# Kernel optimization log

Measured on AMD Instinct MI355X. Metric: run time of the kernel, lower is better.

The kernel has to match this reference:

```python
import jax, jax.numpy as jnp
import numpy as np

N, E = 50000, 800000
IN = OUT = 128
T, R, H = 4, 6, 8
DK = OUT // H


def setup_inputs() -> dict:
    key = jax.random.key(0)
    ks = iter(jax.random.split(key, 24))
    nk = lambda: next(ks)
    return {
        "node_inp": jax.random.normal(nk(), (N, IN), jnp.float32),
        "node_type": jax.random.randint(nk(), (N,), 0, T),
        "edge_index": jax.random.randint(nk(), (2, E), 0, N),
        "edge_type": jax.random.randint(nk(), (E,), 0, R),
        "edge_sign": jax.random.randint(nk(), (E,), -2, 2),
        "edge_distance": jax.random.uniform(nk(), (E,), jnp.float32, 0.0, 2e5),
        "Wq": jax.random.normal(nk(), (T, IN, OUT), jnp.float32) / np.float32(np.sqrt(IN)),
        "bq": jnp.zeros((T, OUT), jnp.float32),
        "Wk": jax.random.normal(nk(), (T, IN, OUT), jnp.float32) / np.float32(np.sqrt(IN)),
        "bk": jnp.zeros((T, OUT), jnp.float32),
        "Wv": jax.random.normal(nk(), (T, IN, OUT), jnp.float32) / np.float32(np.sqrt(IN)),
        "bv": jnp.zeros((T, OUT), jnp.float32),
        "rel_q": jax.random.normal(nk(), (R, H, DK), jnp.float32) * 0.2,
        "rel_k": jax.random.normal(nk(), (R, H, DK), jnp.float32) * 0.2,
        "rel_v": jax.random.normal(nk(), (R, H, DK), jnp.float32) * 0.2,
        "sign_k_neutral": jnp.ones((H, DK), jnp.float32),
        "sign_v_neutral": jnp.ones((H, DK), jnp.float32),
        "rel_bias": jnp.zeros((R, H), jnp.float32),
        "dist_alpha": jnp.asarray(0.5, jnp.float32),
        "dist_tau": jnp.asarray(100000.0, jnp.float32),
        "skip": jnp.ones((T,), jnp.float32),
        "ln_gamma": jnp.ones((T, OUT), jnp.float32),
        "ln_beta": jnp.zeros((T, OUT), jnp.float32),
    }


def reference(node_inp, node_type, edge_index, edge_type, edge_sign, edge_distance,
              Wq, bq, Wk, bk, Wv, bv, rel_q, rel_k, rel_v,
              sign_k_neutral, sign_v_neutral, rel_bias, dist_alpha, dist_tau,
              skip, ln_gamma, ln_beta):
    n = node_inp.shape[0]
    src, dst = edge_index[0], edge_index[1]

    # edge_sign normalization: anything < -1 or == 0 -> -2 (neutral), else clamp to {-1, 1}
    es = jnp.where((edge_sign < -1) | (edge_sign == 0), -2, jnp.clip(edge_sign, -1, 1))
    sign_idx = jnp.where(es == -1, 0, jnp.where(es == 1, 1, 2))  # [E]

    # per-type Q/K/V projections, then select by node_type
    idx = jnp.arange(n)
    Q = (jnp.einsum('ni,tio->tno', node_inp, Wq) + bq[:, None, :])[node_type, idx]
    K = (jnp.einsum('ni,tio->tno', node_inp, Wk) + bk[:, None, :])[node_type, idx]
    V = (jnp.einsum('ni,tio->tno', node_inp, Wv) + bv[:, None, :])[node_type, idx]
    Q = Q.reshape(n, H, DK); K = K.reshape(n, H, DK); V = V.reshape(n, H, DK)

    sign_k_all = jnp.concatenate([-jnp.ones((1, H, DK), Q.dtype), jnp.ones((1, H, DK), Q.dtype), sign_k_neutral[None]], 0)
    sign_v_all = jnp.concatenate([-jnp.ones((1, H, DK), Q.dtype), jnp.ones((1, H, DK), Q.dtype), sign_v_neutral[None]], 0)

    q_eff = Q[dst] * rel_q[edge_type]                        # [E,H,DK]
    k_eff = K[src] * rel_k[edge_type] * sign_k_all[sign_idx]  # [E,H,DK]
    v_eff = V[src] * rel_v[edge_type] * sign_v_all[sign_idx]  # [E,H,DK]

    scores = (q_eff * k_eff).sum(-1) / np.float32(np.sqrt(DK))  # [E,H]
    scores = scores + rel_bias[edge_type]
    phi = dist_alpha * jnp.exp(-edge_distance / (dist_tau + 1e-9))
    scores = scores + phi[:, None]

    # destination-grouped softmax over edges
    m = jax.ops.segment_max(scores, dst, num_segments=n)      # [N,H]
    ex = jnp.exp(scores - m[dst])
    Z = jax.ops.segment_sum(ex, dst, num_segments=n)          # [N,H]
    attn = ex / (Z[dst] + 1e-9)                               # [E,H]

    msg = (v_eff * attn[..., None]).reshape(-1, OUT)          # [E,OUT]
    out = jax.ops.segment_sum(msg, dst, num_segments=n)       # [N,OUT]

    alpha = jax.nn.sigmoid(skip)[node_type][:, None]          # [N,1]
    mix = alpha * out + (1.0 - alpha) * node_inp
    mu = mix.mean(-1, keepdims=True)
    var = ((mix - mu) ** 2).mean(-1, keepdims=True)
    normed = (mix - mu) / jnp.sqrt(var + 1e-5)
    return normed * ln_gamma[node_type] + ln_beta[node_type]
```

## Files before the change

### kernel.cpp

```cpp
#include <hip/hip_runtime.h>

#define N_NODES 50000
#define N_EDGES 800000
#define DIM 128
#define NT 4
#define NR 6
#define NH 8
#define NBLK_SCAN ((N_NODES + 255) / 256)
#define NBLK2 ((N_NODES + 1023) / 1024)
#define NTILE_ROW 3129
#define NPAD_MAX (NTILE_ROW * 16)

#define XCVT_N (N_NODES * DIM / 4)
#define WT_N   (NT * 3 * DIM * DIM)
#define WCB_N  (24 * 32)
#define PREP_TOTAL (XCVT_N + WT_N + WCB_N)
#define PREP_BLOCKS ((PREP_TOTAL + 255) / 256)
#define HIST_BLOCKS (N_EDGES / 256)
#define A_PREP_BASE NBLK_SCAN
#define A_HIST_BASE (NBLK_SCAN + PREP_BLOCKS)
#define A_BLOCKS (A_HIST_BASE + HIST_BLOCKS)

typedef __attribute__((ext_vector_type(8))) short bf16x8;
typedef __attribute__((ext_vector_type(4))) float f32x4;

__device__ __forceinline__ unsigned short f2bf(float f) {
    unsigned int u = __float_as_uint(f);
    return (unsigned short)((u + 0x7fffu + ((u >> 16) & 1u)) >> 16);
}
__device__ __forceinline__ float blo(unsigned int u) { return __uint_as_float(u << 16); }
__device__ __forceinline__ float bhi(unsigned int u) { return __uint_as_float(u & 0xffff0000u); }

__device__ __forceinline__ int sign_index(int s) {
    if (s < -1 || s == 0) return 2;
    return (s == -1) ? 0 : 1;
}

__global__ __launch_bounds__(256) void k_A(
    const int* __restrict__ ntype, int* __restrict__ bhist, int* __restrict__ opad,
    const float* __restrict__ x,
    const float* __restrict__ Wq, const float* __restrict__ Wk, const float* __restrict__ Wv,
    const float* __restrict__ rel_q, const float* __restrict__ rel_k,
    const float* __restrict__ rel_v,
    const float* __restrict__ skn, const float* __restrict__ svn,
    unsigned short* __restrict__ xb, unsigned short* __restrict__ Wt,
    uint4* __restrict__ wcb,
    const int* __restrict__ ei, int* __restrict__ cnt, int* __restrict__ posw)
{
    int blk = blockIdx.x;
    if (blk < NBLK_SCAN) {
        __shared__ int h[NT];
        if (threadIdx.x < NT) h[threadIdx.x] = 0;
        __syncthreads();
        int n = blk * 256 + threadIdx.x;
        if (n < N_NODES) atomicAdd(&h[ntype[n]], 1);
        if (n < NPAD_MAX) opad[n] = -1;
        __syncthreads();
        if (threadIdx.x < NT) bhist[blk * NT + threadIdx.x] = h[threadIdx.x];
        return;
    }
    if (blk < A_HIST_BASE) {
        int i = (blk - A_PREP_BASE) * 256 + threadIdx.x;
        if (i < XCVT_N) {
            float4 v = ((const float4*)x)[i];
            ushort4 o;
            o.x = f2bf(v.x); o.y = f2bf(v.y); o.z = f2bf(v.z); o.w = f2bf(v.w);
            ((ushort4*)xb)[i] = o;
        } else if (i < XCVT_N + WT_N) {
            int j = i - XCVT_N;
            int in = j & 127;
            int b2 = j >> 7;
            int out = b2 & 127;
            int ts = b2 >> 7;
            int sel = ts % 3, t = ts / 3;
            const float* W = sel == 0 ? Wq : (sel == 1 ? Wk : Wv);
            Wt[j] = f2bf(W[((size_t)t * DIM + in) * DIM + out]);
        } else if (i < PREP_TOTAL) {
            int j = i - XCVT_N - WT_N;
            int p = j & 31;
            int cmb = j >> 5;
            int et = cmb & 7, sidx = cmb >> 3;
            if (et < NR) {
                int h2 = p >> 2;
                float wk[4], wv[4];
                #pragma unroll
                for (int q = 0; q < 4; ++q) {
                    int o = 4 * p + q;
                    int rb = (et * NH + h2) * 16 + (o & 15);
                    float sgk = sidx == 0 ? -1.f : (sidx == 1 ? 1.f : skn[o]);
                    float sgv = sidx == 0 ? -1.f : (sidx == 1 ? 1.f : svn[o]);
                    wk[q] = rel_q[rb] * rel_k[rb] * sgk * 0.25f;
                    wv[q] = rel_v[rb] * sgv;
                }
                uint4 u;
                u.x = (unsigned)f2bf(wk[0]) | ((unsigned)f2bf(wk[1]) << 16);
                u.y = (unsigned)f2bf(wv[0]) | ((unsigned)f2bf(wv[1]) << 16);
                u.z = (unsigned)f2bf(wk[2]) | ((unsigned)f2bf(wk[3]) << 16);
                u.w = (unsigned)f2bf(wv[2]) | ((unsigned)f2bf(wv[3]) << 16);
                wcb[cmb * 32 + p] = u;
            }
        }
        return;
    }
    int e = (blk - A_HIST_BASE) * 256 + threadIdx.x;
    if (e < N_EDGES) posw[e] = atomicAdd(&cnt[ei[N_EDGES + e]], 1);
}

__global__ __launch_bounds__(1024) void k_B(
    const int* __restrict__ bhist, int* __restrict__ bbase, int* __restrict__ pb_g,
    const int* __restrict__ cnt, int* __restrict__ offs, int* __restrict__ bsum)
{
    int tid = threadIdx.x;
    if (blockIdx.x == 0) {
        __shared__ int s[1024];
        __shared__ int pb[NT + 1];
        int t = tid / NBLK_SCAN;
        int b = tid - t * NBLK_SCAN;
        int v = (tid < NT * NBLK_SCAN) ? bhist[b * NT + t] : 0;
        s[tid] = v;
        __syncthreads();
        for (int d = 1; d < 1024; d <<= 1) {
            int add = (tid >= d) ? s[tid - d] : 0;
            __syncthreads();
            s[tid] += add;
            __syncthreads();
        }
        if (tid == 0) {
            int acc = 0;
            for (int tt = 0; tt < NT; ++tt) {
                pb[tt] = acc;
                int tot = s[(tt + 1) * NBLK_SCAN - 1] - (tt ? s[tt * NBLK_SCAN - 1] : 0);
                acc += ((tot + 15) >> 4) << 4;
            }
            pb[NT] = acc;
        }
        __syncthreads();
        if (tid < NT * NBLK_SCAN) {
            int excl = s[tid] - v;
            int base_t = t ? s[t * NBLK_SCAN - 1] : 0;
            bbase[b * NT + t] = pb[t] + (excl - base_t);
        }
        if (tid <= NT) pb_g[tid] = pb[tid];
        return;
    }
    int sb = blockIdx.x - 1;
    __shared__ int s[1024];
    int i = sb * 1024 + tid;
    int v = (i < N_NODES) ? cnt[i] : 0;
    s[tid] = v;
    __syncthreads();
    for (int d = 1; d < 1024; d <<= 1) {
        int add = (tid >= d) ? s[tid - d] : 0;
        __syncthreads();
        s[tid] += add;
        __syncthreads();
    }
    if (i < N_NODES) offs[i] = s[tid] - v;
    if (tid == 1023) bsum[sb] = s[1023];
}

__global__ __launch_bounds__(256) void k_C(
    const int* __restrict__ ntype, const int* __restrict__ bbase, int* __restrict__ order_pad,
    const int* __restrict__ bsum, int* __restrict__ bofs, int* __restrict__ offs)
{
    int blk = blockIdx.x;
    if (blk < NBLK_SCAN) {
        __shared__ int cur[NT];
        if (threadIdx.x < NT) cur[threadIdx.x] = bbase[blk * NT + threadIdx.x];
        __syncthreads();
        int n = blk * 256 + threadIdx.x;
        if (n < N_NODES) {
            int t = ntype[n];
            int pos = atomicAdd(&cur[t], 1);
            order_pad[pos] = n;
        }
        return;
    }
    __shared__ int s[256];
    int t = threadIdx.x;
    int v = (t < NBLK2) ? bsum[t] : 0;
    s[t] = v;
    __syncthreads();
    for (int d = 1; d < 256; d <<= 1) {
        int add = (t >= d) ? s[t - d] : 0;
        __syncthreads();
        s[t] += add;
        __syncthreads();
    }
    if (t < NBLK2) {
        int b = s[t] - v;
        bofs[t] = b;
        if (t == NBLK2 - 1) offs[N_NODES] = N_EDGES - b;
    }
}

__global__ __launch_bounds__(256) void k_D(
    const unsigned short* __restrict__ xb, const unsigned short* __restrict__ Wt,
    const int* __restrict__ order_pad, const int* __restrict__ pb_g,
    const float* __restrict__ bq, const float* __restrict__ bk, const float* __restrict__ bv,
    float* __restrict__ Qf, unsigned short* __restrict__ KVu,
    const int* __restrict__ ei, const int* __restrict__ etype,
    const int* __restrict__ esign, const float* __restrict__ edist,
    const float* __restrict__ dalpha, const float* __restrict__ dtau,
    const int* __restrict__ offs, const int* __restrict__ bofs,
    const int* __restrict__ posw, int2* __restrict__ edata)
{
    int b = blockIdx.x;
    if (b >= NTILE_ROW) {
        int e = (b - NTILE_ROW) * 256 + threadIdx.x;
        if (e >= N_EDGES) return;
        int dst = ei[N_EDGES + e];
        int pos = offs[dst] + bofs[dst >> 10] + posw[e];
        int cmb = sign_index(esign[e]) * 8 + etype[e];
        float phi = dalpha[0] * __expf(-edist[e] / (dtau[0] + 1e-9f));
        edata[pos] = make_int2(ei[e] | (cmb << 16), __float_as_int(phi));
        return;
    }
    int row0 = b * 16;
    if (row0 >= pb_g[NT]) return;
    int t = (row0 >= pb_g[3]) ? 3 : (row0 >= pb_g[2]) ? 2 : (row0 >= pb_g[1]) ? 1 : 0;
    int wave = threadIdx.x >> 6, lane = threadIdx.x & 63;
    int arow = row0 + (lane & 15);
    int nidA = order_pad[arow];
    const unsigned short* xrow = xb + (size_t)(nidA < 0 ? 0 : nidA) * DIM;
    int ko = (lane >> 4) * 8;
    bf16x8 afrag[4];
    #pragma unroll
    for (int kt = 0; kt < 4; ++kt) afrag[kt] = *(const bf16x8*)(xrow + kt * 32 + ko);

    #pragma unroll
    for (int g = 0; g < 6; ++g) {
        int ocol = g * 64 + wave * 16 + (lane & 15);
        int sel = ocol >> 7, wcol = ocol & 127;
        const unsigned short* wrow = Wt + ((size_t)(t * 3 + sel) * DIM + wcol) * DIM;
        f32x4 acc = {0.f, 0.f, 0.f, 0.f};
        #pragma unroll
        for (int kt = 0; kt < 4; ++kt) {
            bf16x8 bfr = *(const bf16x8*)(wrow + kt * 32 + ko);
            acc = __builtin_amdgcn_mfma_f32_16x16x32_bf16(afrag[kt], bfr, acc, 0, 0, 0);
        }
        const float* bias_p = sel == 0 ? bq : (sel == 1 ? bk : bv);
        float bias = bias_p[t * DIM + wcol];
        #pragma unroll
        for (int r = 0; r < 4; ++r) {
            int drow = row0 + (lane >> 4) * 4 + r;
            int nid = order_pad[drow];
            if (nid < 0) continue;
            float v = acc[r] + bias;
            if (sel == 0) Qf[(size_t)nid * DIM + wcol] = v;
            else KVu[(size_t)nid * 256 + (wcol >> 1) * 4 + (wcol & 1) + (sel == 2 ? 2 : 0)] = f2bf(v);
        }
    }
}

__global__ __launch_bounds__(256) void k_attn(
    const float4* __restrict__ Qf4, const uint4* __restrict__ KV,
    const uint4* __restrict__ WCB,
    const float* __restrict__ x, const int* __restrict__ ntype,
    const int* __restrict__ offs, const int* __restrict__ bofs,
    const int2* __restrict__ edata,
    const float* __restrict__ rbias, const float* __restrict__ skip,
    const float* __restrict__ gmm, const float* __restrict__ bta,
    float* __restrict__ out)
{
    __shared__ float rb_s[NR * NH];
    if (threadIdx.x < NR * NH) rb_s[threadIdx.x] = rbias[threadIdx.x];
    __syncthreads();
    const int wave = threadIdx.x >> 6, lane = threadIdx.x & 63;
    const int n = blockIdx.x * 4 + wave;
    const int p = lane & 31;
    const int hi = lane >> 5;
    const int h = p >> 2;
    const int beg = offs[n] + bofs[n >> 10];
    const int end = offs[n + 1] + bofs[(n + 1) >> 10];

    const float4 q4 = Qf4[(size_t)n * 32 + p];

    float Z = 0.f, a0 = 0.f, a1 = 0.f, a2 = 0.f, a3 = 0.f;

    auto process = [&](int2 r) {
        int src = r.x & 0xffff;
        unsigned cmb = ((unsigned)r.x) >> 16;
        uint4 kv = KV[(size_t)src * 32 + p];
        uint4 w = WCB[cmb * 32 + p];
        float pp = (q4.x * blo(w.x)) * blo(kv.x);
        pp = fmaf(q4.y * bhi(w.x), bhi(kv.x), pp);
        pp = fmaf(q4.z * blo(w.z), blo(kv.z), pp);
        pp = fmaf(q4.w * bhi(w.z), bhi(kv.z), pp);
        pp += __shfl_xor(pp, 1, 4);
        pp += __shfl_xor(pp, 2, 4);
        float ex = __expf(pp + rb_s[(cmb & 7) * NH + h] + __int_as_float(r.y));
        Z += ex;
        a0 = fmaf(blo(kv.y) * blo(w.y), ex, a0);
        a1 = fmaf(bhi(kv.y) * bhi(w.y), ex, a1);
        a2 = fmaf(blo(kv.w) * blo(w.w), ex, a2);
        a3 = fmaf(bhi(kv.w) * bhi(w.w), ex, a3);
    };

    int rem = end - beg;
    int j = beg;
    if (rem >= 4) {
        int2 r0 = edata[j + hi];
        int2 r1 = edata[j + 2 + hi];
        while (true) {
            int2 c0 = r0, c1 = r1;
            j += 4; rem -= 4;
            if (rem >= 4) { r0 = edata[j + hi]; r1 = edata[j + 2 + hi]; }
            process(c0);
            process(c1);
            if (rem < 4) break;
        }
    }
    while (rem >= 2) {
        int2 c = edata[j + hi];
        process(c);
        j += 2; rem -= 2;
    }
    if (rem) {
        int2 r = edata[j];
        int src = r.x & 0xffff;
        unsigned cmb = ((unsigned)r.x) >> 16;
        uint4 kv = KV[(size_t)src * 32 + p];
        uint4 w = WCB[cmb * 32 + p];
        float pp = (q4.x * blo(w.x)) * blo(kv.x);
        pp = fmaf(q4.y * bhi(w.x), bhi(kv.x), pp);
        pp = fmaf(q4.z * blo(w.z), blo(kv.z), pp);
        pp = fmaf(q4.w * bhi(w.z), bhi(kv.z), pp);
        pp += __shfl_xor(pp, 1, 4);
        pp += __shfl_xor(pp, 2, 4);
        float ex = __expf(pp + rb_s[(cmb & 7) * NH + h] + __int_as_float(r.y));
        ex = hi ? 0.f : ex;
        Z += ex;
        a0 = fmaf(blo(kv.y) * blo(w.y), ex, a0);
        a1 = fmaf(bhi(kv.y) * bhi(w.y), ex, a1);
        a2 = fmaf(blo(kv.w) * blo(w.w), ex, a2);
        a3 = fmaf(bhi(kv.w) * bhi(w.w), ex, a3);
    }

    Z  += __shfl_xor(Z, 32, 64);
    a0 += __shfl_xor(a0, 32, 64);
    a1 += __shfl_xor(a1, 32, 64);
    a2 += __shfl_xor(a2, 32, 64);
    a3 += __shfl_xor(a3, 32, 64);

    float rz = 1.f / (Z + 1e-9f);
    int t = ntype[n];
    float alpha = 1.f / (1.f + __expf(-skip[t]));
    float4 x4 = ((const float4*)x)[(size_t)n * 32 + p];
    float m0 = fmaf(alpha, a0 * rz - x4.x, x4.x);
    float m1 = fmaf(alpha, a1 * rz - x4.y, x4.y);
    float m2 = fmaf(alpha, a2 * rz - x4.z, x4.z);
    float m3 = fmaf(alpha, a3 * rz - x4.w, x4.w);

    float s = (m0 + m1) + (m2 + m3);
    float s2 = fmaf(m0, m0, m1 * m1) + fmaf(m2, m2, m3 * m3);
    #pragma unroll
    for (int d = 32; d >= 1; d >>= 1) {
        s += __shfl_xor(s, d, 64);
        s2 += __shfl_xor(s2, d, 64);
    }
    float mu = s * (1.f / (2 * DIM));
    float var = s2 * (1.f / (2 * DIM)) - mu * mu;
    float rstd = rsqrtf(var + 1e-5f);
    if (hi == 0) {
        float4 g4 = ((const float4*)gmm)[t * 32 + p];
        float4 b4 = ((const float4*)bta)[t * 32 + p];
        float4 o4;
        o4.x = (m0 - mu) * rstd * g4.x + b4.x;
        o4.y = (m1 - mu) * rstd * g4.y + b4.y;
        o4.z = (m2 - mu) * rstd * g4.z + b4.z;
        o4.w = (m3 - mu) * rstd * g4.w + b4.w;
        ((float4*)out)[(size_t)n * 32 + p] = o4;
    }
}

extern "C" void kernel_launch(void* const* d_in, const int* in_sizes, int n_in,
                              void* d_out, int out_size, void* d_ws, size_t ws_size,
                              hipStream_t stream) {
    const float* x      = (const float*)d_in[0];
    const int*   ntype  = (const int*)d_in[1];
    const int*   ei     = (const int*)d_in[2];
    const int*   etype  = (const int*)d_in[3];
    const int*   esign  = (const int*)d_in[4];
    const float* edist  = (const float*)d_in[5];
    const float* Wq     = (const float*)d_in[6];
    const float* bq     = (const float*)d_in[7];
    const float* Wk     = (const float*)d_in[8];
    const float* bk     = (const float*)d_in[9];
    const float* Wv     = (const float*)d_in[10];
    const float* bv     = (const float*)d_in[11];
    const float* rel_q  = (const float*)d_in[12];
    const float* rel_k  = (const float*)d_in[13];
    const float* rel_v  = (const float*)d_in[14];
    const float* skn    = (const float*)d_in[15];
    const float* svn    = (const float*)d_in[16];
    const float* rbias  = (const float*)d_in[17];
    const float* dalpha = (const float*)d_in[18];
    const float* dtau   = (const float*)d_in[19];
    const float* skip   = (const float*)d_in[20];
    const float* gmm    = (const float*)d_in[21];
    const float* bta    = (const float*)d_in[22];
    float* out = (float*)d_out;

    char* ws = (char*)d_ws;
    float*          Qf     = (float*)         (ws + 0);
    unsigned short* KVu    = (unsigned short*)(ws + 25600000);
    unsigned short* xb     = (unsigned short*)(ws + 51200000);
    unsigned short* Wt     = (unsigned short*)(ws + 64000000);
    uint4*          wcb    = (uint4*)         (ws + 64500000);
    int*            cnt    = (int*)           (ws + 64600000);
    int*            offs   = (int*)           (ws + 64900000);
    int*            bsum   = (int*)           (ws + 65200000);
    int*            bofs   = (int*)           (ws + 65210000);
    int*            posw   = (int*)           (ws + 65300000);
    int2*           edata  = (int2*)          (ws + 68600000);
    int*            opad   = (int*)           (ws + 75000000);
    int*            bhist  = (int*)           (ws + 75300000);
    int*            bbase  = (int*)           (ws + 75310000);
    int*            pb     = (int*)           (ws + 75320000);

    hipMemsetAsync(cnt, 0, (size_t)N_NODES * 4, stream);
    k_A <<<A_BLOCKS, 256, 0, stream>>>(ntype, bhist, opad,
                                       x, Wq, Wk, Wv, rel_q, rel_k, rel_v, skn, svn,
                                       xb, Wt, wcb, ei, cnt, posw);
    k_B <<<1 + NBLK2, 1024, 0, stream>>>(bhist, bbase, pb, cnt, offs, bsum);
    k_C <<<NBLK_SCAN + 1, 256, 0, stream>>>(ntype, bbase, opad, bsum, bofs, offs);
    k_D <<<NTILE_ROW + HIST_BLOCKS, 256, 0, stream>>>(xb, Wt, opad, pb, bq, bk, bv,
                                                      Qf, KVu,
                                                      ei, etype, esign, edist, dalpha, dtau,
                                                      offs, bofs, posw, edata);
    k_attn <<<N_NODES / 4, 256, 0, stream>>>((const float4*)Qf, (const uint4*)KVu,
                                             (const uint4*)wcb, x, ntype, offs, bofs,
                                             edata, rbias, skip, gmm, bta, out);
}
```

Baseline: 175.3 us.

## Store Q/K/V in type-sorted slot order and remap edge sources to slots

Q and KV rows are now stored at their padded type-sorted slot position instead of the original node id. This lets k_D write KV tiles contiguously through an LDS staging buffer with coalesced 16-byte stores, rather than scattering 2-byte writes. Edge records now carry the source's slot index via a new slot[] lookup, and k_attn reads Q through slot[n]. The cost is an extra indirection per edge in preprocessing, one more per node in attention, and a reshuffled workspace layout.

```diff
diff --git a/kernel.cpp b/kernel.cpp
--- a/kernel.cpp
+++ b/kernel.cpp
@@ -161,6 +161,7 @@
 
 __global__ __launch_bounds__(256) void k_C(
     const int* __restrict__ ntype, const int* __restrict__ bbase, int* __restrict__ order_pad,
+    int* __restrict__ slot,
     const int* __restrict__ bsum, int* __restrict__ bofs, int* __restrict__ offs)
 {
     int blk = blockIdx.x;
@@ -173,6 +174,7 @@
             int t = ntype[n];
             int pos = atomicAdd(&cur[t], 1);
             order_pad[pos] = n;
+            slot[n] = pos;
         }
         return;
     }
@@ -199,6 +201,7 @@
     const int* __restrict__ order_pad, const int* __restrict__ pb_g,
     const float* __restrict__ bq, const float* __restrict__ bk, const float* __restrict__ bv,
     float* __restrict__ Qf, unsigned short* __restrict__ KVu,
+    const int* __restrict__ slot,
     const int* __restrict__ ei, const int* __restrict__ etype,
     const int* __restrict__ esign, const float* __restrict__ edist,
     const float* __restrict__ dalpha, const float* __restrict__ dtau,
@@ -213,7 +216,8 @@
         int pos = offs[dst] + bofs[dst >> 10] + posw[e];
         int cmb = sign_index(esign[e]) * 8 + etype[e];
         float phi = dalpha[0] * __expf(-edist[e] / (dtau[0] + 1e-9f));
-        edata[pos] = make_int2(ei[e] | (cmb << 16), __float_as_int(phi));
+        int sslot = slot[ei[e]];
+        edata[pos] = make_int2(sslot | (cmb << 16), __float_as_int(phi));
         return;
     }
     int row0 = b * 16;
@@ -228,6 +232,7 @@
     #pragma unroll
     for (int kt = 0; kt < 4; ++kt) afrag[kt] = *(const bf16x8*)(xrow + kt * 32 + ko);
 
+    __shared__ unsigned short kvt[16 * 256];
     #pragma unroll
     for (int g = 0; g < 6; ++g) {
         int ocol = g * 64 + wave * 16 + (lane & 15);
@@ -243,20 +248,24 @@
         float bias = bias_p[t * DIM + wcol];
         #pragma unroll
         for (int r = 0; r < 4; ++r) {
-            int drow = row0 + (lane >> 4) * 4 + r;
-            int nid = order_pad[drow];
-            if (nid < 0) continue;
+            int lrow = (lane >> 4) * 4 + r;
             float v = acc[r] + bias;
-            if (sel == 0) Qf[(size_t)nid * DIM + wcol] = v;
-            else KVu[(size_t)nid * 256 + (wcol >> 1) * 4 + (wcol & 1) + (sel == 2 ? 2 : 0)] = f2bf(v);
-        }
-    }
+            if (sel == 0) Qf[(size_t)(row0 + lrow) * DIM + wcol] = v;
+            else kvt[lrow * 256 + (wcol >> 1) * 4 + (wcol & 1) + (sel == 2 ? 2 : 0)] = f2bf(v);
+        }
+    }
+    __syncthreads();
+    const uint4* s4 = (const uint4*)kvt;
+    uint4* d4 = (uint4*)KVu + (size_t)row0 * 32;
+    d4[threadIdx.x] = s4[threadIdx.x];
+    d4[256 + threadIdx.x] = s4[256 + threadIdx.x];
 }
 
 __global__ __launch_bounds__(256) void k_attn(
     const float4* __restrict__ Qf4, const uint4* __restrict__ KV,
     const uint4* __restrict__ WCB,
     const float* __restrict__ x, const int* __restrict__ ntype,
+    const int* __restrict__ slot,
     const int* __restrict__ offs, const int* __restrict__ bofs,
     const int2* __restrict__ edata,
     const float* __restrict__ rbias, const float* __restrict__ skip,
@@ -274,7 +283,8 @@
     const int beg = offs[n] + bofs[n >> 10];
     const int end = offs[n + 1] + bofs[(n + 1) >> 10];
 
-    const float4 q4 = Qf4[(size_t)n * 32 + p];
+    const int sl = slot[n];
+    const float4 q4 = Qf4[(size_t)sl * 32 + p];
 
     float Z = 0.f, a0 = 0.f, a1 = 0.f, a2 = 0.f, a3 = 0.f;
 
@@ -404,32 +414,33 @@
 
     char* ws = (char*)d_ws;
     float*          Qf     = (float*)         (ws + 0);
-    unsigned short* KVu    = (unsigned short*)(ws + 25600000);
-    unsigned short* xb     = (unsigned short*)(ws + 51200000);
-    unsigned short* Wt     = (unsigned short*)(ws + 64000000);
-    uint4*          wcb    = (uint4*)         (ws + 64500000);
-    int*            cnt    = (int*)           (ws + 64600000);
+    unsigned short* KVu    = (unsigned short*)(ws + 25700000);
+    unsigned short* xb     = (unsigned short*)(ws + 51400000);
+    unsigned short* Wt     = (unsigned short*)(ws + 64200000);
+    uint4*          wcb    = (uint4*)         (ws + 64600000);
+    int*            cnt    = (int*)           (ws + 64700000);
     int*            offs   = (int*)           (ws + 64900000);
     int*            bsum   = (int*)           (ws + 65200000);
     int*            bofs   = (int*)           (ws + 65210000);
     int*            posw   = (int*)           (ws + 65300000);
     int2*           edata  = (int2*)          (ws + 68600000);
     int*            opad   = (int*)           (ws + 75000000);
-    int*            bhist  = (int*)           (ws + 75300000);
-    int*            bbase  = (int*)           (ws + 75310000);
-    int*            pb     = (int*)           (ws + 75320000);
+    int*            slot   = (int*)           (ws + 75220000);
+    int*            bhist  = (int*)           (ws + 75450000);
+    int*            bbase  = (int*)           (ws + 75460000);
+    int*            pb     = (int*)           (ws + 75470000);
 
     hipMemsetAsync(cnt, 0, (size_t)N_NODES * 4, stream);
     k_A <<<A_BLOCKS, 256, 0, stream>>>(ntype, bhist, opad,
                                        x, Wq, Wk, Wv, rel_q, rel_k, rel_v, skn, svn,
                                        xb, Wt, wcb, ei, cnt, posw);
     k_B <<<1 + NBLK2, 1024, 0, stream>>>(bhist, bbase, pb, cnt, offs, bsum);
-    k_C <<<NBLK_SCAN + 1, 256, 0, stream>>>(ntype, bbase, opad, bsum, bofs, offs);
+    k_C <<<NBLK_SCAN + 1, 256, 0, stream>>>(ntype, bbase, opad, slot, bsum, bofs, offs);
     k_D <<<NTILE_ROW + HIST_BLOCKS, 256, 0, stream>>>(xb, Wt, opad, pb, bq, bk, bv,
-                                                      Qf, KVu,
+                                                      Qf, KVu, slot,
                                                       ei, etype, esign, edist, dalpha, dtau,
                                                       offs, bofs, posw, edata);
     k_attn <<<N_NODES / 4, 256, 0, stream>>>((const float4*)Qf, (const uint4*)KVu,
-                                             (const uint4*)wcb, x, ntype, offs, bofs,
+                                             (const uint4*)wcb, x, ntype, slot, offs, bofs,
                                              edata, rbias, skip, gmm, bta, out);
 }
```

Result: slower. 185.8 us (+6.0%).
